# Kernel optimization log

Hardware: AMD Instinct MI355X
Metric: run time of the kernel (lower is better)

## Reference

```python
import jax, jax.numpy as jnp
import numpy as np
from jax import lax

BN_EPS = 1e-5


def _condconv(x, w, b, fc_w, fc_b):
    """CondConv2D: per-sample expert mixing then 3x3 conv (pad=1, stride=1).
    x: [B, Cin, H, W]; w: [E, Cout, Cin, 3, 3]; b: [Cout]; fc_w: [E, Cin]; fc_b: [E].
    """
    B, Cin, H, W = x.shape
    E, Cout, _, kh, kw = w.shape
    pooled = x.mean(axis=(2, 3))                               # [B, Cin] adaptive_avg_pool2d(1,1)+flatten
    rw = jax.nn.sigmoid(pooled @ fc_w.T + fc_b)                # [B, E] routing weights
    kernels = jnp.einsum('be,eoihw->boihw', rw, w)             # [B, Cout, Cin, 3, 3]
    # Batched per-sample conv via grouped conv: groups = B
    xi = x.reshape(1, B * Cin, H, W)
    ker = kernels.reshape(B * Cout, Cin, kh, kw)
    out = lax.conv_general_dilated(
        xi, ker, window_strides=(1, 1), padding=((1, 1), (1, 1)),
        feature_group_count=B,
        dimension_numbers=('NCHW', 'OIHW', 'NCHW'))
    return out.reshape(B, Cout, H, W) + b[None, :, None, None]


def _bn_relu(x, g, b, m, v):
    # eval-mode BatchNorm2d followed by ReLU
    inv = g * lax.rsqrt(v + BN_EPS)
    return jax.nn.relu(x * inv[None, :, None, None] + (b - m * inv)[None, :, None, None])


def setup_inputs() -> dict:
    key = jax.random.key(0)
    ks = jax.random.split(key, 8)
    B, Cin, Cout, H, W, E = 16, 64, 128, 128, 128, 3
    s1 = 1.0 / np.sqrt(Cin * 9)
    s2 = 1.0 / np.sqrt(Cout * 9)
    return {
        'x': jax.random.normal(ks[0], (B, Cin, H, W), jnp.float32),
        'w1': jax.random.normal(ks[1], (E, Cout, Cin, 3, 3), jnp.float32) * s1,
        'b1': jax.random.normal(ks[2], (Cout,), jnp.float32) * s1,
        'fc1_w': jax.random.normal(ks[3], (E, Cin), jnp.float32) / np.sqrt(Cin),
        'fc1_b': jnp.zeros((E,), jnp.float32),
        'bn1_g': jnp.ones((Cout,), jnp.float32),
        'bn1_b': jnp.zeros((Cout,), jnp.float32),
        'bn1_m': jnp.zeros((Cout,), jnp.float32),
        'bn1_v': jnp.ones((Cout,), jnp.float32),
        'w2': jax.random.normal(ks[4], (E, Cout, Cout, 3, 3), jnp.float32) * s2,
        'b2': jax.random.normal(ks[5], (Cout,), jnp.float32) * s2,
        'fc2_w': jax.random.normal(ks[6], (E, Cout), jnp.float32) / np.sqrt(Cout),
        'fc2_b': jnp.zeros((E,), jnp.float32),
        'bn2_g': jnp.ones((Cout,), jnp.float32),
        'bn2_b': jnp.zeros((Cout,), jnp.float32),
        'bn2_m': jnp.zeros((Cout,), jnp.float32),
        'bn2_v': jnp.ones((Cout,), jnp.float32),
    }


def reference(x, w1, b1, fc1_w, fc1_b, bn1_g, bn1_b, bn1_m, bn1_v,
              w2, b2, fc2_w, fc2_b, bn2_g, bn2_b, bn2_m, bn2_v):
    h = _condconv(x, w1, b1, fc1_w, fc1_b)
    h = _bn_relu(h, bn1_g, bn1_b, bn1_m, bn1_v)
    h = _condconv(h, w2, b2, fc2_w, fc2_b)
    h = _bn_relu(h, bn2_g, bn2_b, bn2_m, bn2_v)
    return h
```

## Files before the change

### kernel.cpp

```cpp
#include <hip/hip_runtime.h>
#include <math.h>

#define BN_EPS 1e-5f

typedef short bf16x8 __attribute__((ext_vector_type(8)));
typedef float f32x4 __attribute__((ext_vector_type(4)));
typedef float f32x16 __attribute__((ext_vector_type(16)));
typedef unsigned short ushort8v __attribute__((ext_vector_type(8)));
typedef unsigned int uint;
typedef unsigned short ushort;

__device__ inline ushort f2bf(float f) {
    uint u = __float_as_uint(f);
    uint r = u + 0x7FFFu + ((u >> 16) & 1u);
    return (ushort)(r >> 16);
}
__device__ inline float bf2f(ushort u) { return __uint_as_float(((uint)u) << 16); }
__device__ inline uint cvtpk(float lo, float hi) {
    uint r;
    asm("v_cvt_pk_bf16_f32 %0, %1, %2" : "=v"(r) : "v"(lo), "v"(hi));
    return r;
}

__global__ void scsh_kernel(const float* b1, const float* g1, const float* bb1,
                            const float* m1, const float* v1,
                            const float* b2, const float* g2, const float* bb2,
                            const float* m2, const float* v2,
                            float* scsh1, float* scsh2) {
    int t = threadIdx.x;
    if (t < 128) {
        float sc = g1[t] * rsqrtf(v1[t] + BN_EPS);
        scsh1[t] = sc;
        scsh1[128 + t] = (b1[t] - m1[t]) * sc + bb1[t];
    } else {
        int c = t - 128;
        float sc = g2[c] * rsqrtf(v2[c] + BN_EPS);
        scsh2[c] = sc;
        scsh2[128 + c] = (b2[c] - m2[c]) * sc + bb2[c];
    }
}

__global__ void xprep_kernel(const float* __restrict__ x, ushort* __restrict__ xT,
                             float* __restrict__ pooled1) {
    __shared__ float t[64][65];
    const int b = blockIdx.y;
    const int p0 = blockIdx.x * 64;
    const int tid = threadIdx.x;
#pragma unroll
    for (int it = 0; it < 16; ++it) {
        const int idx = it * 256 + tid;
        const int ci = idx >> 6, p = idx & 63;
        t[ci][p] = x[((size_t)b * 64 + ci) * 16384 + p0 + p];
    }
    __syncthreads();
    const int h = p0 >> 7;
#pragma unroll
    for (int it = 0; it < 2; ++it) {
        const int p = it * 32 + (tid >> 3);
        const int w = (p0 & 127) + p;
        const int c0 = (tid & 7) * 8;
        const int cc = c0 >> 4;
        ushort8v u;
#pragma unroll
        for (int j = 0; j < 8; ++j) u[j] = f2bf(t[c0 + j][p]);
        *(ushort8v*)&xT[(((size_t)(b * 128 + h) * 4 + cc) * 128 + w) * 16 + (c0 & 15)] = u;
    }
    if (tid < 64) {
        float s = 0.f;
#pragma unroll 8
        for (int p = 0; p < 64; ++p) s += t[tid][p];
        atomicAdd(&pooled1[b * 64 + tid], s);
    }
}

__global__ void pool2h_kernel(const ushort* __restrict__ hT, float* __restrict__ pooled2) {
    const int b = blockIdx.x, slab = blockIdx.y;
    const int tid = threadIdx.x;
    const int cc = tid >> 5, o = (tid >> 4) & 1, wb = tid & 15;
    float a[8] = {0.f, 0.f, 0.f, 0.f, 0.f, 0.f, 0.f, 0.f};
    for (int r = 0; r < 4; ++r) {
        const int h = slab * 4 + r;
        const ushort* base = hT + ((size_t)(b * 128 + h) * 8 + cc) * 2048 + o * 8;
#pragma unroll
        for (int k = 0; k < 8; ++k) {
            const ushort8v u = *(const ushort8v*)(base + (wb + k * 16) * 16);
#pragma unroll
            for (int j = 0; j < 8; ++j) a[j] += bf2f(u[j]);
        }
    }
    __shared__ float sp[16][8][17];
    const int grp0 = cc * 2 + o;
#pragma unroll
    for (int j = 0; j < 8; ++j) sp[grp0][j][wb] = a[j];
    __syncthreads();
    if (tid < 128) {
        const int grp = tid >> 3, j = tid & 7;
        float s = 0.f;
#pragma unroll
        for (int k = 0; k < 16; ++k) s += sp[grp][j][k];
        const int c = (grp >> 1) * 16 + (grp & 1) * 8 + j;
        atomicAdd(&pooled2[b * 128 + c], s);
    }
}

template <int CIN>
__global__ void mix_route_kernel(const float* __restrict__ w, const float* __restrict__ pooled,
                                 const float* __restrict__ fcw, const float* __restrict__ fcb,
                                 ushort* __restrict__ wmix) {
    constexpr int NCC = CIN / 16;
    __shared__ float rwl[48];
    const int tid = threadIdx.x;
    if (tid < 48) {
        const int bb = tid / 3, e = tid % 3;
        float d = 0.f;
        for (int c = 0; c < CIN; ++c) d += pooled[bb * CIN + c] * fcw[e * CIN + c];
        const float s = fcb[e] + d * (1.f / 16384.f);
        rwl[tid] = 1.f / (1.f + expf(-s));
    }
    __syncthreads();
    const int co = blockIdx.x;
    for (int b = 0; b < 16; ++b) {
        const float r0 = rwl[b * 3 + 0], r1 = rwl[b * 3 + 1], r2 = rwl[b * 3 + 2];
        for (int idx = tid; idx < CIN * 9; idx += 256) {
            const int ci = idx & (CIN - 1);
            const int tap = idx / CIN;
            const size_t off = ((size_t)co * CIN + ci) * 9 + tap;
            const float m = r0 * w[off]
                          + r1 * w[off + (size_t)128 * CIN * 9]
                          + r2 * w[off + (size_t)2 * 128 * CIN * 9];
            const int cc = ci >> 4, o = (ci >> 3) & 1, e = ci & 7;
            const size_t dst = ((size_t)(b * NCC + cc) * 2304
                             + tap * 256 + o * 128 + co) * 8 + e;
            wmix[dst] = f2bf(m);
        }
    }
}

template <int CIN, bool TO_BF16>
__global__ __launch_bounds__(1024, 4)
void conv_mfma11_kernel(const ushort* __restrict__ xT, const ushort* __restrict__ wmix,
                        const float* __restrict__ scsh,
                        float* __restrict__ outf, ushort* __restrict__ outh) {
    constexpr int NCC = CIN / 16;
    constexpr int IBUF = 24960;
    constexpr int WOFF = 2 * IBUF;
    constexpr int WBUF = 36864;
    __shared__ __align__(16) char smem[123648];

    const int L = ((blockIdx.x & 7) << 6) | (blockIdx.x >> 3);
    const int b = L >> 5;
    const int rt = L & 31;

    const int tid = threadIdx.x;
    const int lane = tid & 63, wid = tid >> 6;
    const int wm = wid >> 3;
    const int rp = (wid >> 2) & 1;
    const int cb = wid & 3;
    const int l31 = lane & 31, lhi = lane >> 5;

    f32x16 acc[2][2];
#pragma unroll
    for (int i = 0; i < 2; ++i)
#pragma unroll
        for (int j = 0; j < 2; ++j)
#pragma unroll
            for (int r = 0; r < 16; ++r) acc[i][j][r] = 0.f;

    const ushort* inb = xT + (size_t)b * 128 * NCC * 2048;
    const ushort* wmb = wmix + (size_t)b * NCC * 18432;

    const int ihalf = wid & 1, ioct = (wid >> 1) & 1, ir0 = (wid & 15) >> 2;
    const int iv = (ihalf * 64 + lane) * 16 + ioct * 8;
    const int idst0 = (ir0 * 260 + ioct * 130 + 1 + ihalf * 64) * 16;
    const int hg0 = rt * 4 - 1 + ir0;
    const int wo0 = wid * 512 + lane * 8;
    const int wd0 = wid * 1024 + lane * 16;

    auto stage = [&](char* dI, char* dW, int cc) {
        const size_t ccI = (size_t)cc * 2048;
        if ((unsigned)hg0 < 128u) {
            const ushort* src = inb + (size_t)hg0 * (NCC * 2048) + ccI + iv;
            __builtin_amdgcn_global_load_lds(
                (const __attribute__((address_space(1))) void*)src,
                (__attribute__((address_space(3))) void*)(dI + idst0),
                16, 0, 0);
        }
        if (wid < 8) {
            const int hg = hg0 + 4;
            if ((unsigned)hg < 128u) {
                const ushort* src = inb + (size_t)hg * (NCC * 2048) + ccI + iv;
                __builtin_amdgcn_global_load_lds(
                    (const __attribute__((address_space(1))) void*)src,
                    (__attribute__((address_space(3))) void*)(dI + idst0 + 4 * 4160),
                    16, 0, 0);
            }
        }
        const ushort* ws = wmb + (size_t)cc * 18432;
#pragma unroll
        for (int u = 0; u < 2; ++u) {
            __builtin_amdgcn_global_load_lds(
                (const __attribute__((address_space(1))) void*)(ws + wo0 + u * 8192),
                (__attribute__((address_space(3))) void*)(dW + wd0 + u * 16384),
                16, 0, 0);
        }
        if (wid < 4) {
            __builtin_amdgcn_global_load_lds(
                (const __attribute__((address_space(1))) void*)(ws + wo0 + 16384),
                (__attribute__((address_space(3))) void*)(dW + wd0 + 32768),
                16, 0, 0);
        }
    };

    const int ibase = (rp * 2 * 260 + lhi * 130 + cb * 32 + l31) * 16;
    const int wbase = (lhi * 128 + wm * 64 + l31) * 16;
    const char* pI0 = smem + ibase;
    const char* pI1 = smem + IBUF + ibase;
    const char* pW0 = smem + WOFF + wbase;
    const char* pW1 = smem + WOFF + WBUF + wbase;

    auto taps = [&](const char* pI, const char* pW) {
        bf16x8 rb0[3], rb1[3];
#pragma unroll
        for (int dx = 0; dx < 3; ++dx) {
            rb0[dx] = *(const bf16x8*)(pI + (0 * 260 + dx) * 16);
            rb1[dx] = *(const bf16x8*)(pI + (1 * 260 + dx) * 16);
        }
#pragma unroll
        for (int dy = 0; dy < 3; ++dy) {
#pragma unroll
            for (int dx = 0; dx < 3; ++dx) {
                const int tap = dy * 3 + dx;
                const bf16x8 af0 = *(const bf16x8*)(pW + (tap * 256) * 16);
                const bf16x8 af1 = *(const bf16x8*)(pW + (tap * 256 + 32) * 16);
                acc[0][0] = __builtin_amdgcn_mfma_f32_32x32x16_bf16(af0, rb0[dx], acc[0][0], 0, 0, 0);
                acc[1][0] = __builtin_amdgcn_mfma_f32_32x32x16_bf16(af1, rb0[dx], acc[1][0], 0, 0, 0);
                acc[0][1] = __builtin_amdgcn_mfma_f32_32x32x16_bf16(af0, rb1[dx], acc[0][1], 0, 0, 0);
                acc[1][1] = __builtin_amdgcn_mfma_f32_32x32x16_bf16(af1, rb1[dx], acc[1][1], 0, 0, 0);
            }
            if (dy < 2) {
#pragma unroll
                for (int dx = 0; dx < 3; ++dx) {
                    rb0[dx] = rb1[dx];
                    rb1[dx] = *(const bf16x8*)(pI + ((dy + 2) * 260 + dx) * 16);
                }
            }
        }
    };

    if (tid < 48) {
        const int bi = tid >= 24, idx = tid - bi * 24;
        const int r = idx >> 2, j = idx & 3;
        const int g = r * 260 + (j >> 1) * 130 + (j & 1) * 129;
        *(f32x4*)(smem + bi * IBUF + g * 16) = f32x4{0.f, 0.f, 0.f, 0.f};
    }
    if (rt == 0 || rt == 31) {
        const int r = (rt == 0) ? 0 : 5;
        if (tid < 520) {
            const int bi = tid >= 260, gr = tid - bi * 260;
            *(f32x4*)(smem + bi * IBUF + (r * 260 + gr) * 16) = f32x4{0.f, 0.f, 0.f, 0.f};
        }
    }

    stage(smem, smem + WOFF, 0);
    asm volatile("s_waitcnt vmcnt(0)" ::: "memory");
    __syncthreads();

    for (int cc = 0; cc < NCC; cc += 2) {
        stage(smem + IBUF, smem + WOFF + WBUF, cc + 1);
        __builtin_amdgcn_sched_barrier(0);
        taps(pI0, pW0);
        __syncthreads();
        if (cc + 2 < NCC) stage(smem, smem + WOFF, cc + 2);
        __builtin_amdgcn_sched_barrier(0);
        taps(pI1, pW1);
        __syncthreads();
    }

    if constexpr (!TO_BF16) {
#pragma unroll
        for (int mf = 0; mf < 2; ++mf) {
            const int cob = wm * 64 + mf * 32 + 4 * lhi;
            f32x4 sc[4], sh[4];
#pragma unroll
            for (int q = 0; q < 4; ++q) {
                sc[q] = *(const f32x4*)&scsh[cob + 8 * q];
                sh[q] = *(const f32x4*)&scsh[128 + cob + 8 * q];
            }
#pragma unroll
            for (int nf = 0; nf < 2; ++nf) {
                const size_t pbase = (size_t)(rt * 4 + rp * 2 + nf) * 128 + cb * 32 + l31;
#pragma unroll
                for (int q = 0; q < 4; ++q)
#pragma unroll
                    for (int s = 0; s < 4; ++s) {
                        float y = fmaf(acc[mf][nf][q * 4 + s], sc[q][s], sh[q][s]);
                        y = y > 0.f ? y : 0.f;
                        outf[((size_t)(b * 128 + cob + 8 * q + s)) * 16384 + pbase] = y;
                    }
            }
        }
    } else {
        ushort* sf = (ushort*)smem;
#pragma unroll
        for (int p = 0; p < 2; ++p) {
            if (rp == p) {
#pragma unroll
                for (int mf = 0; mf < 2; ++mf)
#pragma unroll
                    for (int q = 0; q < 4; ++q) {
                        const int co4 = wm * 64 + mf * 32 + 8 * q + 4 * lhi;
                        const f32x4 sc = *(const f32x4*)&scsh[co4];
                        const f32x4 sh = *(const f32x4*)&scsh[128 + co4];
#pragma unroll
                        for (int nf = 0; nf < 2; ++nf) {
                            const int px = nf * 128 + cb * 32 + l31;
                            float v[4];
#pragma unroll
                            for (int s = 0; s < 4; ++s) {
                                float y = fmaf(acc[mf][nf][q * 4 + s], sc[s], sh[s]);
                                v[s] = y > 0.f ? y : 0.f;
                            }
                            uint2 pk;
                            pk.x = cvtpk(v[0], v[1]);
                            pk.y = cvtpk(v[2], v[3]);
                            *(uint2*)&sf[px * 136 + co4] = pk;
                        }
                    }
            }
            __syncthreads();
#pragma unroll
            for (int it = 0; it < 2; ++it) {
                const int id = it * 1024 + tid;
                const int lr = id >> 10, cc = (id >> 7) & 7, w = id & 127;
                const uint4 v0 = *(const uint4*)&sf[(lr * 128 + w) * 136 + cc * 16];
                const uint4 v1 = *(const uint4*)&sf[(lr * 128 + w) * 136 + cc * 16 + 8];
                ushort* dst = outh + (((size_t)(b * 128 + rt * 4 + 2 * p + lr)) * 8 + cc) * 2048 + w * 16;
                *(uint4*)dst = v0;
                *(uint4*)(dst + 8) = v1;
            }
            if (p == 0) __syncthreads();
        }
    }
}

extern "C" void kernel_launch(void* const* d_in, const int* in_sizes, int n_in,
                              void* d_out, int out_size, void* d_ws, size_t ws_size,
                              hipStream_t stream) {
    const float* x     = (const float*)d_in[0];
    const float* w1    = (const float*)d_in[1];
    const float* b1    = (const float*)d_in[2];
    const float* fc1_w = (const float*)d_in[3];
    const float* fc1_b = (const float*)d_in[4];
    const float* bn1g  = (const float*)d_in[5];
    const float* bn1b  = (const float*)d_in[6];
    const float* bn1m  = (const float*)d_in[7];
    const float* bn1v  = (const float*)d_in[8];
    const float* w2    = (const float*)d_in[9];
    const float* b2    = (const float*)d_in[10];
    const float* fc2_w = (const float*)d_in[11];
    const float* fc2_b = (const float*)d_in[12];
    const float* bn2g  = (const float*)d_in[13];
    const float* bn2b  = (const float*)d_in[14];
    const float* bn2m  = (const float*)d_in[15];
    const float* bn2v  = (const float*)d_in[16];

    float* out = (float*)d_out;
    char* ws = (char*)d_ws;

    ushort* hT    = (ushort*)(ws + 0);
    ushort* xT    = (ushort*)(ws + 67108864);
    ushort* wmix1 = (ushort*)(ws + 100663296);
    ushort* wmix2 = (ushort*)(ws + 103022592);
    float*  pool1 = (float*) (ws + 107741184);
    float*  pool2 = (float*) (ws + 107745280);
    float*  scsh1 = (float*) (ws + 107753472);
    float*  scsh2 = (float*) (ws + 107754496);

    hipMemsetAsync(pool1, 0, 4096, stream);
    hipMemsetAsync(pool2, 0, 8192, stream);

    scsh_kernel<<<1, 256, 0, stream>>>(b1, bn1g, bn1b, bn1m, bn1v,
                                       b2, bn2g, bn2b, bn2m, bn2v, scsh1, scsh2);

    xprep_kernel<<<dim3(256, 16), 256, 0, stream>>>(x, xT, pool1);
    mix_route_kernel<64><<<128, 256, 0, stream>>>(w1, pool1, fc1_w, fc1_b, wmix1);
    conv_mfma11_kernel<64, true><<<512, 1024, 0, stream>>>(
        xT, wmix1, scsh1, nullptr, hT);

    pool2h_kernel<<<dim3(16, 32), 256, 0, stream>>>(hT, pool2);
    mix_route_kernel<128><<<128, 256, 0, stream>>>(w2, pool2, fc2_w, fc2_b, wmix2);
    conv_mfma11_kernel<128, false><<<512, 1024, 0, stream>>>(
        hT, wmix2, scsh2, out, nullptr);
}
```

Before: 204.1 us.

## Make conv staging uniform per wave and use counted waits with raw barriers

The conv kernel's global-to-LDS staging is restructured so that every wave issues exactly four async loads per chunk. Out-of-range rows and spare slots are redirected to a trash LDS region instead of being skipped, which allows a fixed s_waitcnt vmcnt(4). The loop replaces __syncthreads with explicit counted waits and s_barrier, fully unrolls it, and raises wave priority around the MFMA tap sections. The aim is to let the next chunk's prefetch stay in flight while the current chunk computes, at the cost of some redundant loads and extra LDS.

After: 205.9 us. No clear change (+0.9%).

```diff
diff --git a/kernel.cpp b/kernel.cpp
--- a/kernel.cpp
+++ b/kernel.cpp
@@ -138,14 +138,15 @@
 
 template <int CIN, bool TO_BF16>
 __global__ __launch_bounds__(1024, 4)
-void conv_mfma11_kernel(const ushort* __restrict__ xT, const ushort* __restrict__ wmix,
+void conv_mfma12_kernel(const ushort* __restrict__ xT, const ushort* __restrict__ wmix,
                         const float* __restrict__ scsh,
                         float* __restrict__ outf, ushort* __restrict__ outh) {
     constexpr int NCC = CIN / 16;
     constexpr int IBUF = 24960;
     constexpr int WOFF = 2 * IBUF;
     constexpr int WBUF = 36864;
-    __shared__ __align__(16) char smem[123648];
+    constexpr int TRASH = 2 * IBUF + 2 * WBUF;
+    __shared__ __align__(16) char smem[123648 + 1024];
 
     const int L = ((blockIdx.x & 7) << 6) | (blockIdx.x >> 3);
     const int b = L >> 5;
@@ -173,41 +174,42 @@
     const int iv = (ihalf * 64 + lane) * 16 + ioct * 8;
     const int idst0 = (ir0 * 260 + ioct * 130 + 1 + ihalf * 64) * 16;
     const int hg0 = rt * 4 - 1 + ir0;
-    const int wo0 = wid * 512 + lane * 8;
-    const int wd0 = wid * 1024 + lane * 16;
-
-    auto stage = [&](char* dI, char* dW, int cc) {
+    const bool ok0 = (unsigned)hg0 < 128u;
+    const bool ok4 = (unsigned)(hg0 + 4) < 128u;
+    const int wkA = 2 * wid, wkB = 2 * wid + 1;
+    const int wkC = 24 + wid;
+    char* const trash = smem + TRASH;
+
+    auto stage4 = [&](char* dI, char* dW, int cc) {
         const size_t ccI = (size_t)cc * 2048;
-        if ((unsigned)hg0 < 128u) {
-            const ushort* src = inb + (size_t)hg0 * (NCC * 2048) + ccI + iv;
+        {
+            const ushort* src = inb + (ok0 ? (size_t)hg0 * (NCC * 2048) : 0) + ccI + iv;
+            void* dst = ok0 ? (void*)(dI + idst0) : (void*)trash;
             __builtin_amdgcn_global_load_lds(
                 (const __attribute__((address_space(1))) void*)src,
-                (__attribute__((address_space(3))) void*)(dI + idst0),
-                16, 0, 0);
-        }
+                (__attribute__((address_space(3))) void*)dst, 16, 0, 0);
+        }
+        const ushort* ws = wmb + (size_t)cc * 18432;
+        __builtin_amdgcn_global_load_lds(
+            (const __attribute__((address_space(1))) void*)(ws + wkA * 512 + lane * 8),
+            (__attribute__((address_space(3))) void*)(dW + wkA * 1024), 16, 0, 0);
+        __builtin_amdgcn_global_load_lds(
+            (const __attribute__((address_space(1))) void*)(ws + wkB * 512 + lane * 8),
+            (__attribute__((address_space(3))) void*)(dW + wkB * 1024), 16, 0, 0);
         if (wid < 8) {
-            const int hg = hg0 + 4;
-            if ((unsigned)hg < 128u) {
-                const ushort* src = inb + (size_t)hg * (NCC * 2048) + ccI + iv;
-                __builtin_amdgcn_global_load_lds(
-                    (const __attribute__((address_space(1))) void*)src,
-                    (__attribute__((address_space(3))) void*)(dI + idst0 + 4 * 4160),
-                    16, 0, 0);
-            }
-        }
-        const ushort* ws = wmb + (size_t)cc * 18432;
-#pragma unroll
-        for (int u = 0; u < 2; ++u) {
+            const ushort* src = inb + (ok4 ? (size_t)(hg0 + 4) * (NCC * 2048) : 0) + ccI + iv;
+            void* dst = ok4 ? (void*)(dI + idst0 + 4 * 4160) : (void*)trash;
             __builtin_amdgcn_global_load_lds(
-                (const __attribute__((address_space(1))) void*)(ws + wo0 + u * 8192),
-                (__attribute__((address_space(3))) void*)(dW + wd0 + u * 16384),
-                16, 0, 0);
-        }
-        if (wid < 4) {
+                (const __attribute__((address_space(1))) void*)src,
+                (__attribute__((address_space(3))) void*)dst, 16, 0, 0);
+        } else if (wid < 12) {
             __builtin_amdgcn_global_load_lds(
-                (const __attribute__((address_space(1))) void*)(ws + wo0 + 16384),
-                (__attribute__((address_space(3))) void*)(dW + wd0 + 32768),
-                16, 0, 0);
+                (const __attribute__((address_space(1))) void*)(ws + wkC * 512 + lane * 8),
+                (__attribute__((address_space(3))) void*)(dW + wkC * 1024), 16, 0, 0);
+        } else {
+            __builtin_amdgcn_global_load_lds(
+                (const __attribute__((address_space(1))) void*)(ws + lane * 8),
+                (__attribute__((address_space(3))) void*)trash, 16, 0, 0);
         }
     };
 
@@ -261,20 +263,35 @@
         }
     }
 
-    stage(smem, smem + WOFF, 0);
-    asm volatile("s_waitcnt vmcnt(0)" ::: "memory");
-    __syncthreads();
-
+    stage4(smem, smem + WOFF, 0);
+    asm volatile("s_waitcnt vmcnt(0) lgkmcnt(0)" ::: "memory");
+    __builtin_amdgcn_s_barrier();
+
+#pragma unroll
     for (int cc = 0; cc < NCC; cc += 2) {
-        stage(smem + IBUF, smem + WOFF + WBUF, cc + 1);
+        stage4(smem + IBUF, smem + WOFF + WBUF, cc + 1);
+        asm volatile("s_waitcnt vmcnt(4)" ::: "memory");
         __builtin_amdgcn_sched_barrier(0);
+        __builtin_amdgcn_s_barrier();
+        __builtin_amdgcn_s_setprio(1);
         taps(pI0, pW0);
-        __syncthreads();
-        if (cc + 2 < NCC) stage(smem, smem + WOFF, cc + 2);
+        __builtin_amdgcn_s_setprio(0);
+        __builtin_amdgcn_s_barrier();
+
+        if (cc + 2 < NCC) {
+            stage4(smem, smem + WOFF, cc + 2);
+            asm volatile("s_waitcnt vmcnt(4)" ::: "memory");
+        } else {
+            asm volatile("s_waitcnt vmcnt(0)" ::: "memory");
+        }
         __builtin_amdgcn_sched_barrier(0);
+        __builtin_amdgcn_s_barrier();
+        __builtin_amdgcn_s_setprio(1);
         taps(pI1, pW1);
-        __syncthreads();
-    }
+        __builtin_amdgcn_s_setprio(0);
+        __builtin_amdgcn_s_barrier();
+    }
+    __builtin_amdgcn_sched_barrier(0);
 
     if constexpr (!TO_BF16) {
 #pragma unroll
@@ -384,11 +401,11 @@
 
     xprep_kernel<<<dim3(256, 16), 256, 0, stream>>>(x, xT, pool1);
     mix_route_kernel<64><<<128, 256, 0, stream>>>(w1, pool1, fc1_w, fc1_b, wmix1);
-    conv_mfma11_kernel<64, true><<<512, 1024, 0, stream>>>(
+    conv_mfma12_kernel<64, true><<<512, 1024, 0, stream>>>(
         xT, wmix1, scsh1, nullptr, hT);
 
     pool2h_kernel<<<dim3(16, 32), 256, 0, stream>>>(hT, pool2);
     mix_route_kernel<128><<<128, 256, 0, stream>>>(w2, pool2, fc2_w, fc2_b, wmix2);
-    conv_mfma11_kernel<128, false><<<512, 1024, 0, stream>>>(
+    conv_mfma12_kernel<128, false><<<512, 1024, 0, stream>>>(
         hT, wmix2, scsh2, out, nullptr);
 }
```

## Interleave staging loads with per-row MFMA phases and raise wave priority

Applied to the files above, without the earlier changes.

Splits each channel-chunk's conv taps into three dy phases separated by workgroup barriers. The next chunk's global-to-LDS loads are split into two halves and issued between those phases, and MFMA bursts are wrapped in s_setprio to favour math waves. The aim is to spread memory issue across the compute window and keep all waves in lockstep so LDS reads and MFMAs overlap better. It adds extra barriers per chunk and moves the vmcnt wait to the end of each chunk, which may add sync stalls.

After: 204.7 us. Within noise of the previous version (+0.3%).

```diff
diff --git a/kernel.cpp b/kernel.cpp
--- a/kernel.cpp
+++ b/kernel.cpp
@@ -138,7 +138,7 @@
 
 template <int CIN, bool TO_BF16>
 __global__ __launch_bounds__(1024, 4)
-void conv_mfma11_kernel(const ushort* __restrict__ xT, const ushort* __restrict__ wmix,
+void conv_mfma13_kernel(const ushort* __restrict__ xT, const ushort* __restrict__ wmix,
                         const float* __restrict__ scsh,
                         float* __restrict__ outf, ushort* __restrict__ outh) {
     constexpr int NCC = CIN / 16;
@@ -173,41 +173,40 @@
     const int iv = (ihalf * 64 + lane) * 16 + ioct * 8;
     const int idst0 = (ir0 * 260 + ioct * 130 + 1 + ihalf * 64) * 16;
     const int hg0 = rt * 4 - 1 + ir0;
+    const bool ok0 = (unsigned)hg0 < 128u;
+    const bool ok4 = (wid < 8) && ((unsigned)(hg0 + 4) < 128u);
     const int wo0 = wid * 512 + lane * 8;
     const int wd0 = wid * 1024 + lane * 16;
 
-    auto stage = [&](char* dI, char* dW, int cc) {
+    auto stageA = [&](char* dI, char* dW, int cc) {
         const size_t ccI = (size_t)cc * 2048;
-        if ((unsigned)hg0 < 128u) {
+        if (ok0) {
             const ushort* src = inb + (size_t)hg0 * (NCC * 2048) + ccI + iv;
             __builtin_amdgcn_global_load_lds(
                 (const __attribute__((address_space(1))) void*)src,
-                (__attribute__((address_space(3))) void*)(dI + idst0),
-                16, 0, 0);
-        }
-        if (wid < 8) {
-            const int hg = hg0 + 4;
-            if ((unsigned)hg < 128u) {
-                const ushort* src = inb + (size_t)hg * (NCC * 2048) + ccI + iv;
-                __builtin_amdgcn_global_load_lds(
-                    (const __attribute__((address_space(1))) void*)src,
-                    (__attribute__((address_space(3))) void*)(dI + idst0 + 4 * 4160),
-                    16, 0, 0);
-            }
+                (__attribute__((address_space(3))) void*)(dI + idst0), 16, 0, 0);
         }
         const ushort* ws = wmb + (size_t)cc * 18432;
-#pragma unroll
-        for (int u = 0; u < 2; ++u) {
+        __builtin_amdgcn_global_load_lds(
+            (const __attribute__((address_space(1))) void*)(ws + wo0),
+            (__attribute__((address_space(3))) void*)(dW + wd0), 16, 0, 0);
+    };
+    auto stageB = [&](char* dI, char* dW, int cc) {
+        const size_t ccI = (size_t)cc * 2048;
+        if (ok4) {
+            const ushort* src = inb + (size_t)(hg0 + 4) * (NCC * 2048) + ccI + iv;
             __builtin_amdgcn_global_load_lds(
-                (const __attribute__((address_space(1))) void*)(ws + wo0 + u * 8192),
-                (__attribute__((address_space(3))) void*)(dW + wd0 + u * 16384),
-                16, 0, 0);
-        }
+                (const __attribute__((address_space(1))) void*)src,
+                (__attribute__((address_space(3))) void*)(dI + idst0 + 4 * 4160), 16, 0, 0);
+        }
+        const ushort* ws = wmb + (size_t)cc * 18432;
+        __builtin_amdgcn_global_load_lds(
+            (const __attribute__((address_space(1))) void*)(ws + wo0 + 8192),
+            (__attribute__((address_space(3))) void*)(dW + wd0 + 16384), 16, 0, 0);
         if (wid < 4) {
             __builtin_amdgcn_global_load_lds(
                 (const __attribute__((address_space(1))) void*)(ws + wo0 + 16384),
-                (__attribute__((address_space(3))) void*)(dW + wd0 + 32768),
-                16, 0, 0);
+                (__attribute__((address_space(3))) void*)(dW + wd0 + 32768), 16, 0, 0);
         }
     };
 
@@ -218,33 +217,57 @@
     const char* pW0 = smem + WOFF + wbase;
     const char* pW1 = smem + WOFF + WBUF + wbase;
 
-    auto taps = [&](const char* pI, const char* pW) {
-        bf16x8 rb0[3], rb1[3];
+    auto mfma_dy = [&](const char* pW, int dy, const bf16x8* rlo, const bf16x8* rhi) {
+#pragma unroll
+        for (int dx = 0; dx < 3; ++dx) {
+            const int tap = dy * 3 + dx;
+            const bf16x8 af0 = *(const bf16x8*)(pW + (tap * 256) * 16);
+            const bf16x8 af1 = *(const bf16x8*)(pW + (tap * 256 + 32) * 16);
+            acc[0][0] = __builtin_amdgcn_mfma_f32_32x32x16_bf16(af0, rlo[dx], acc[0][0], 0, 0, 0);
+            acc[1][0] = __builtin_amdgcn_mfma_f32_32x32x16_bf16(af1, rlo[dx], acc[1][0], 0, 0, 0);
+            acc[0][1] = __builtin_amdgcn_mfma_f32_32x32x16_bf16(af0, rhi[dx], acc[0][1], 0, 0, 0);
+            acc[1][1] = __builtin_amdgcn_mfma_f32_32x32x16_bf16(af1, rhi[dx], acc[1][1], 0, 0, 0);
+        }
+    };
+
+    auto chunk3 = [&](const char* pI, const char* pW, char* dIn, char* dWn,
+                      int ccn, bool doStage) {
+        bf16x8 rb0[3], rb1[3], rb2[3];
 #pragma unroll
         for (int dx = 0; dx < 3; ++dx) {
             rb0[dx] = *(const bf16x8*)(pI + (0 * 260 + dx) * 16);
             rb1[dx] = *(const bf16x8*)(pI + (1 * 260 + dx) * 16);
         }
-#pragma unroll
-        for (int dy = 0; dy < 3; ++dy) {
-#pragma unroll
-            for (int dx = 0; dx < 3; ++dx) {
-                const int tap = dy * 3 + dx;
-                const bf16x8 af0 = *(const bf16x8*)(pW + (tap * 256) * 16);
-                const bf16x8 af1 = *(const bf16x8*)(pW + (tap * 256 + 32) * 16);
-                acc[0][0] = __builtin_amdgcn_mfma_f32_32x32x16_bf16(af0, rb0[dx], acc[0][0], 0, 0, 0);
-                acc[1][0] = __builtin_amdgcn_mfma_f32_32x32x16_bf16(af1, rb0[dx], acc[1][0], 0, 0, 0);
-                acc[0][1] = __builtin_amdgcn_mfma_f32_32x32x16_bf16(af0, rb1[dx], acc[0][1], 0, 0, 0);
-                acc[1][1] = __builtin_amdgcn_mfma_f32_32x32x16_bf16(af1, rb1[dx], acc[1][1], 0, 0, 0);
-            }
-            if (dy < 2) {
-#pragma unroll
-                for (int dx = 0; dx < 3; ++dx) {
-                    rb0[dx] = rb1[dx];
-                    rb1[dx] = *(const bf16x8*)(pI + ((dy + 2) * 260 + dx) * 16);
-                }
-            }
-        }
+        if (doStage) stageA(dIn, dWn, ccn);
+        __builtin_amdgcn_s_barrier();
+        asm volatile("s_waitcnt lgkmcnt(0)" ::: "memory");
+        __builtin_amdgcn_sched_barrier(0);
+        __builtin_amdgcn_s_setprio(1);
+        mfma_dy(pW, 0, rb0, rb1);
+        __builtin_amdgcn_s_setprio(0);
+        __builtin_amdgcn_s_barrier();
+#pragma unroll
+        for (int dx = 0; dx < 3; ++dx)
+            rb2[dx] = *(const bf16x8*)(pI + (2 * 260 + dx) * 16);
+        if (doStage) stageB(dIn, dWn, ccn);
+        __builtin_amdgcn_s_barrier();
+        asm volatile("s_waitcnt lgkmcnt(0)" ::: "memory");
+        __builtin_amdgcn_sched_barrier(0);
+        __builtin_amdgcn_s_setprio(1);
+        mfma_dy(pW, 1, rb1, rb2);
+        __builtin_amdgcn_s_setprio(0);
+        __builtin_amdgcn_s_barrier();
+#pragma unroll
+        for (int dx = 0; dx < 3; ++dx)
+            rb0[dx] = *(const bf16x8*)(pI + (3 * 260 + dx) * 16);
+        __builtin_amdgcn_s_barrier();
+        asm volatile("s_waitcnt lgkmcnt(0)" ::: "memory");
+        __builtin_amdgcn_sched_barrier(0);
+        __builtin_amdgcn_s_setprio(1);
+        mfma_dy(pW, 2, rb2, rb0);
+        __builtin_amdgcn_s_setprio(0);
+        if (doStage) asm volatile("s_waitcnt vmcnt(0)" ::: "memory");
+        __builtin_amdgcn_s_barrier();
     };
 
     if (tid < 48) {
@@ -261,20 +284,16 @@
         }
     }
 
-    stage(smem, smem + WOFF, 0);
-    asm volatile("s_waitcnt vmcnt(0)" ::: "memory");
-    __syncthreads();
+    stageA(smem, smem + WOFF, 0);
+    stageB(smem, smem + WOFF, 0);
+    asm volatile("s_waitcnt vmcnt(0) lgkmcnt(0)" ::: "memory");
+    __builtin_amdgcn_s_barrier();
 
     for (int cc = 0; cc < NCC; cc += 2) {
-        stage(smem + IBUF, smem + WOFF + WBUF, cc + 1);
-        __builtin_amdgcn_sched_barrier(0);
-        taps(pI0, pW0);
-        __syncthreads();
-        if (cc + 2 < NCC) stage(smem, smem + WOFF, cc + 2);
-        __builtin_amdgcn_sched_barrier(0);
-        taps(pI1, pW1);
-        __syncthreads();
-    }
+        chunk3(pI0, pW0, smem + IBUF, smem + WOFF + WBUF, cc + 1, true);
+        chunk3(pI1, pW1, smem, smem + WOFF, cc + 2, cc + 2 < NCC);
+    }
+    __builtin_amdgcn_sched_barrier(0);
 
     if constexpr (!TO_BF16) {
 #pragma unroll
@@ -384,11 +403,11 @@
 
     xprep_kernel<<<dim3(256, 16), 256, 0, stream>>>(x, xT, pool1);
     mix_route_kernel<64><<<128, 256, 0, stream>>>(w1, pool1, fc1_w, fc1_b, wmix1);
-    conv_mfma11_kernel<64, true><<<512, 1024, 0, stream>>>(
+    conv_mfma13_kernel<64, true><<<512, 1024, 0, stream>>>(
         xT, wmix1, scsh1, nullptr, hT);
 
     pool2h_kernel<<<dim3(16, 32), 256, 0, stream>>>(hT, pool2);
     mix_route_kernel<128><<<128, 256, 0, stream>>>(w2, pool2, fc2_w, fc2_b, wmix2);
-    conv_mfma11_kernel<128, false><<<512, 1024, 0, stream>>>(
+    conv_mfma13_kernel<128, false><<<512, 1024, 0, stream>>>(
         hT, wmix2, scsh2, out, nullptr);
 }
```
